# Optimization experiments

Measured on AMD Instinct MI355X. Metric: run time of the kernel, lower is better.

The kernel has to match this reference:

```python
import jax, jax.numpy as jnp
import numpy as np

D_MODEL = 1024
N_HEAD = 16
HEAD_DIM = D_MODEL // N_HEAD


def setup_inputs() -> dict:
    key = jax.random.key(0)
    k1, k2, k3 = jax.random.split(key, 3)
    B, T = 2, 2048
    x = jax.random.normal(k1, (B, T, D_MODEL), dtype=jnp.float32)
    # nn.MultiheadAttention packed in-projection: (3*D, D), xavier-like scale
    w_in = jax.random.normal(k2, (3 * D_MODEL, D_MODEL), dtype=jnp.float32) * (1.0 / np.sqrt(D_MODEL))
    b_in = jnp.zeros((3 * D_MODEL,), dtype=jnp.float32)
    w_out = jax.random.normal(k3, (D_MODEL, D_MODEL), dtype=jnp.float32) * (1.0 / np.sqrt(D_MODEL))
    b_out = jnp.zeros((D_MODEL,), dtype=jnp.float32)
    return {"x": x, "w_in": w_in, "b_in": b_in, "w_out": w_out, "b_out": b_out}


def reference(x, w_in, b_in, w_out, b_out):
    B, T, D = x.shape
    H, hd = N_HEAD, HEAD_DIM
    # packed QKV projection (torch Linear convention: y = x @ W.T + b)
    qkv = x @ w_in.T + b_in                      # [B, T, 3D]
    q, k, v = jnp.split(qkv, 3, axis=-1)
    # [B, H, T, hd]
    q = q.reshape(B, T, H, hd).transpose(0, 2, 1, 3)
    k = k.reshape(B, T, H, hd).transpose(0, 2, 1, 3)
    v = v.reshape(B, T, H, hd).transpose(0, 2, 1, 3)
    scale = 1.0 / np.sqrt(hd).astype(np.float32)
    scores = jnp.einsum("bhqd,bhkd->bhqk", q * scale, k)  # [B, H, T, T]
    causal = jnp.tril(jnp.ones((T, T), dtype=bool))
    scores = jnp.where(causal, scores, jnp.finfo(scores.dtype).min)
    attn = jax.nn.softmax(scores, axis=-1)
    ctx = jnp.einsum("bhqk,bhkd->bhqd", attn, v)           # [B, H, T, hd]
    ctx = ctx.transpose(0, 2, 1, 3).reshape(B, T, D)
    return ctx @ w_out.T + b_out
```

## Files before the change

### kernel.cpp

```cpp
#include <hip/hip_runtime.h>


#define T_SEQ 2048
#define D_MODEL 1024
#define NEG_BIG (-1.0e30f)
#define Q_SCALE 0.18033688f

typedef float f32x4 __attribute__((ext_vector_type(4)));
typedef short s16x8 __attribute__((ext_vector_type(8)));
typedef __bf16 bf16x8 __attribute__((ext_vector_type(8)));

__device__ __forceinline__ f32x4 mfma16(s16x8 a, s16x8 b, f32x4 c) {
    return __builtin_amdgcn_mfma_f32_16x16x32_bf16(
        __builtin_bit_cast(bf16x8, a), __builtin_bit_cast(bf16x8, b), c, 0, 0, 0);
}

__device__ __forceinline__ short f2bf(float f) {
    unsigned int u = __float_as_uint(f);
    u += 0x7fffu + ((u >> 16) & 1u);
    return (short)(u >> 16);
}
__device__ __forceinline__ unsigned f2bfu(float f) {
    unsigned int u = __float_as_uint(f);
    u += 0x7fffu + ((u >> 16) & 1u);
    return u >> 16;
}
__device__ __forceinline__ unsigned f2bfu_fast(float f) {
    return (__float_as_uint(f) + 0x8000u) >> 16;
}
__device__ __forceinline__ float bf2f(short s) {
    return __uint_as_float(((unsigned int)(unsigned short)s) << 16);
}

__device__ __forceinline__ void async_lds16(const short* g, short* l) {
    __builtin_amdgcn_global_load_lds(
        (const __attribute__((address_space(1))) unsigned int*)g,
        (__attribute__((address_space(3))) unsigned int*)l, 16, 0, 0);
}

#define N_X   4194304
#define N_WI  3145728
#define N_BI  3072
#define N_WO  1048576
#define N_BO  1024
#define V_X   (N_X  / 4)
#define V_WI  (N_WI / 4)
#define V_BI  (N_BI / 4)
#define V_WO  (N_WO / 4)
#define V_BO  (N_BO / 4)
#define V_TOT (V_X + V_WI + V_BI + V_WO + V_BO)

__global__ __launch_bounds__(256) void canon_all_kernel(
    const float* __restrict__ x, const float* __restrict__ wi,
    const float* __restrict__ bi, const float* __restrict__ wo,
    const float* __restrict__ bo,
    short* __restrict__ xb, short* __restrict__ wib, short* __restrict__ bib,
    short* __restrict__ wob, short* __restrict__ bob)
{
    int i = blockIdx.x * 256 + threadIdx.x;
    if (i >= V_TOT) return;
    const float* src; short* dst; int off;
    if      (i < V_X)                    { src = x;  dst = xb;  off = i; }
    else if (i < V_X+V_WI)               { src = wi; dst = wib; off = i - V_X; }
    else if (i < V_X+V_WI+V_BI)          { src = bi; dst = bib; off = i - V_X - V_WI; }
    else if (i < V_X+V_WI+V_BI+V_WO)     { src = wo; dst = wob; off = i - V_X - V_WI - V_BI; }
    else                                 { src = bo; dst = bob; off = i - V_X - V_WI - V_BI - V_WO; }
    float4 v = ((const float4*)src)[off];
    short4 o = { f2bf(v.x), f2bf(v.y), f2bf(v.z), f2bf(v.w) };
    ((short4*)dst)[off] = o;
}

__global__ __launch_bounds__(256) void gemm_qkv_kernel(
    const short* __restrict__ A, const short* __restrict__ B,
    const short* __restrict__ bias,
    short* __restrict__ qo, short* __restrict__ ko, short* __restrict__ vto)
{
    const int K = 1024;
    alignas(16) __shared__ short As[128][32];
    alignas(16) __shared__ short Bs[128][32];
    const int m0 = blockIdx.x * 128;
    const int n0 = blockIdx.y * 128;
    const int tid = threadIdx.x;
    const int lane = tid & 63;
    const int w = tid >> 6;
    const int wm = (w >> 1) * 64, wn = (w & 1) * 64;
    const int quad = lane >> 4, l16 = lane & 15;

    f32x4 acc[4][4];
    const f32x4 zero = {0.f, 0.f, 0.f, 0.f};
#pragma unroll
    for (int i = 0; i < 4; ++i)
#pragma unroll
        for (int j = 0; j < 4; ++j) acc[i][j] = zero;

    const int lrow = lane >> 2;
    const int lcol = (lane & 3) * 8;
    const short* gA0 = &A[(m0 + w*32      + lrow) * K + lcol];
    const short* gA1 = &A[(m0 + w*32 + 16 + lrow) * K + lcol];
    const short* gB0 = &B[(n0 + w*32      + lrow) * K + lcol];
    const short* gB1 = &B[(n0 + w*32 + 16 + lrow) * K + lcol];
    short* lA0 = &As[w*32][0];
    short* lA1 = &As[w*32 + 16][0];
    short* lB0 = &Bs[w*32][0];
    short* lB1 = &Bs[w*32 + 16][0];

    for (int k0 = 0; k0 < K; k0 += 32) {
        __syncthreads();
        async_lds16(gA0 + k0, lA0);
        async_lds16(gA1 + k0, lA1);
        async_lds16(gB0 + k0, lB0);
        async_lds16(gB1 + k0, lB1);
        __syncthreads();

        s16x8 af[4], bfr[4];
#pragma unroll
        for (int i = 0; i < 4; ++i) af[i]  = *(const s16x8*)&As[wm + i*16 + l16][quad*8];
#pragma unroll
        for (int j = 0; j < 4; ++j) bfr[j] = *(const s16x8*)&Bs[wn + j*16 + l16][quad*8];
#pragma unroll
        for (int i = 0; i < 4; ++i)
#pragma unroll
            for (int j = 0; j < 4; ++j)
                acc[i][j] = mfma16(af[i], bfr[j], acc[i][j]);
    }

#pragma unroll
    for (int j = 0; j < 4; ++j) {
        int n = n0 + wn + j*16 + l16;
        float bi = bf2f(bias[n]);
        int which = n >> 10;
        int h = (n >> 6) & 15, d = n & 63;
        if (which < 2) {
            short* dst = (which == 0) ? qo : ko;
            float scl = (which == 0) ? Q_SCALE : 1.0f;
#pragma unroll
            for (int i = 0; i < 4; ++i) {
#pragma unroll
                for (int r = 0; r < 4; ++r) {
                    int m = m0 + wm + i*16 + quad*4 + r;
                    int b = m >> 11, t = m & 2047;
                    float v = (acc[i][j][r] + bi) * scl;
                    dst[(((b*16 + h) * 2048) + t) * 64 + d] = f2bf(v);
                }
            }
        } else {
#pragma unroll
            for (int i = 0; i < 4; ++i) {
                int m = m0 + wm + i*16 + quad*4;
                int b = m >> 11, t0 = m & 2047;
                short4 o4 = { f2bf(acc[i][j][0] + bi), f2bf(acc[i][j][1] + bi),
                              f2bf(acc[i][j][2] + bi), f2bf(acc[i][j][3] + bi) };
                *(short4*)&vto[(((size_t)(b*16 + h) * 64) + d) * 2048 + t0] = o4;
            }
        }
    }
}

__global__ __launch_bounds__(256) void attn_kernel(
    const short* __restrict__ Q, const short* __restrict__ K,
    const short* __restrict__ Vt, short* __restrict__ ctx)
{
    alignas(16) __shared__ short Ks[64][72];
    alignas(16) __shared__ short Vs[64][72];
    alignas(16) __shared__ short Pl[4][16][72];

    const int id = blockIdx.x;
    const int kk = id >> 8;
    const int r8 = id & 255;
    const int a  = r8 & 15;
    const int bhl = r8 >> 4;
    int qt, bh;
    if      (kk == 0) { qt = a;      bh = bhl;      }
    else if (kk == 1) { qt = 31 - a; bh = bhl;      }
    else if (kk == 2) { qt = 15 - a; bh = 16 + bhl; }
    else              { qt = 16 + a; bh = 16 + bhl; }

    const int qbase = qt * 64;
    const int tid = threadIdx.x;
    const int w = tid >> 6, lane = tid & 63;
    const int quad = lane >> 4, l16 = lane & 15;
    const int b = bh >> 4, h = bh & 15;

    const short* Qb  = Q  + bh * T_SEQ * 64;
    const short* Kb  = K  + bh * T_SEQ * 64;
    const short* Vbt = Vt + (size_t)bh * 64 * T_SEQ;

    const short* qrow = Qb + (qbase + w*16 + l16) * 64;
    const s16x8 qa0 = *(const s16x8*)(qrow + quad*8);
    const s16x8 qa1 = *(const s16x8*)(qrow + 32 + quad*8);

    const f32x4 zero = {0.f, 0.f, 0.f, 0.f};
    f32x4 o[4];
#pragma unroll
    for (int dt = 0; dt < 4; ++dt) o[dt] = zero;
    float lsum = 0.f;

    const int sr  = tid >> 3;
    const int scl = (tid & 7) * 8;
    const int qg  = qbase + w*16 + l16;

    float4 kf0 = *(const float4*)&Kb[sr * 64 + scl];
    float4 kf1 = *(const float4*)&Kb[(sr + 32) * 64 + scl];
    float4 vf0 = *(const float4*)&Vbt[(size_t)sr * T_SEQ + scl];
    float4 vf1 = *(const float4*)&Vbt[(size_t)(sr + 32) * T_SEQ + scl];

    for (int s0 = 0; s0 <= qbase; s0 += 64) {
        __syncthreads();
        *(float4*)&Ks[sr][scl]    = kf0;
        *(float4*)&Ks[sr+32][scl] = kf1;
        *(float4*)&Vs[sr][scl]    = vf0;
        *(float4*)&Vs[sr+32][scl] = vf1;
        __syncthreads();

        if (s0 + 64 <= qbase) {
            kf0 = *(const float4*)&Kb[(s0 + 64 + sr) * 64 + scl];
            kf1 = *(const float4*)&Kb[(s0 + 64 + sr + 32) * 64 + scl];
            vf0 = *(const float4*)&Vbt[(size_t)sr * T_SEQ + s0 + 64 + scl];
            vf1 = *(const float4*)&Vbt[(size_t)(sr + 32) * T_SEQ + s0 + 64 + scl];
        }

#pragma unroll
        for (int sub = 0; sub < 4; ++sub) {
            s16x8 ka0 = *(const s16x8*)&Ks[sub*16 + l16][quad*8];
            s16x8 ka1 = *(const s16x8*)&Ks[sub*16 + l16][32 + quad*8];
            f32x4 S = mfma16(ka1, qa1, mfma16(ka0, qa0, zero));
            if (s0 == qbase) {
                int sb = s0 + sub*16 + quad*4;
#pragma unroll
                for (int r = 0; r < 4; ++r)
                    if (sb + r > qg) S[r] = NEG_BIG;
            }
            float p0 = exp2f(S[0]), p1 = exp2f(S[1]);
            float p2 = exp2f(S[2]), p3 = exp2f(S[3]);
            lsum += (p0 + p1) + (p2 + p3);
            uint2 pk;
            pk.x = f2bfu_fast(p0) | (f2bfu_fast(p1) << 16);
            pk.y = f2bfu_fast(p2) | (f2bfu_fast(p3) << 16);
            *(uint2*)&Pl[w][l16][sub*16 + quad*4] = pk;
        }

        s16x8 pb0 = *(const s16x8*)&Pl[w][l16][quad*8];
        s16x8 pb1 = *(const s16x8*)&Pl[w][l16][32 + quad*8];
#pragma unroll
        for (int dt = 0; dt < 4; ++dt) {
            s16x8 va0 = *(const s16x8*)&Vs[dt*16 + l16][quad*8];
            s16x8 va1 = *(const s16x8*)&Vs[dt*16 + l16][32 + quad*8];
            o[dt] = mfma16(va1, pb1, mfma16(va0, pb0, o[dt]));
        }
    }

    lsum += __shfl_xor(lsum, 16, 64);
    lsum += __shfl_xor(lsum, 32, 64);
    float inv = 1.0f / lsum;
    int base = (b * T_SEQ + qg) * D_MODEL + h * 64;
#pragma unroll
    for (int dt = 0; dt < 4; ++dt) {
        uint2 pk;
        pk.x = f2bfu(o[dt][0] * inv) | (f2bfu(o[dt][1] * inv) << 16);
        pk.y = f2bfu(o[dt][2] * inv) | (f2bfu(o[dt][3] * inv) << 16);
        *(uint2*)&ctx[base + dt*16 + quad*4] = pk;
    }
}

__global__ __launch_bounds__(256) void gemm_out_kernel(
    const short* __restrict__ A, const short* __restrict__ B,
    const short* __restrict__ bias, float* __restrict__ out)
{
    const int K = 1024;
    alignas(16) __shared__ short As[128][32];
    alignas(16) __shared__ short Bs[64][32];
    const int m0 = blockIdx.x * 128;
    const int n0 = blockIdx.y * 64;
    const int tid = threadIdx.x;
    const int lane = tid & 63;
    const int w = tid >> 6;
    const int wm = (w >> 1) * 64, wn = (w & 1) * 32;
    const int quad = lane >> 4, l16 = lane & 15;

    f32x4 acc[4][2];
    const f32x4 zero = {0.f, 0.f, 0.f, 0.f};
#pragma unroll
    for (int i = 0; i < 4; ++i)
#pragma unroll
        for (int j = 0; j < 2; ++j) acc[i][j] = zero;

    const int lrow = lane >> 2;
    const int lcol = (lane & 3) * 8;
    const short* gA0 = &A[(m0 + w*32      + lrow) * K + lcol];
    const short* gA1 = &A[(m0 + w*32 + 16 + lrow) * K + lcol];
    const short* gB0 = &B[(n0 + w*16 + lrow) * K + lcol];
    short* lA0 = &As[w*32][0];
    short* lA1 = &As[w*32 + 16][0];
    short* lB0 = &Bs[w*16][0];

    for (int k0 = 0; k0 < K; k0 += 32) {
        __syncthreads();
        async_lds16(gA0 + k0, lA0);
        async_lds16(gA1 + k0, lA1);
        async_lds16(gB0 + k0, lB0);
        __syncthreads();

        s16x8 af[4], bfr[2];
#pragma unroll
        for (int i = 0; i < 4; ++i) af[i]  = *(const s16x8*)&As[wm + i*16 + l16][quad*8];
#pragma unroll
        for (int j = 0; j < 2; ++j) bfr[j] = *(const s16x8*)&Bs[wn + j*16 + l16][quad*8];
#pragma unroll
        for (int i = 0; i < 4; ++i)
#pragma unroll
            for (int j = 0; j < 2; ++j)
                acc[i][j] = mfma16(af[i], bfr[j], acc[i][j]);
    }

#pragma unroll
    for (int j = 0; j < 2; ++j) {
        int n = n0 + wn + j*16 + l16;
        float bi = bf2f(bias[n]);
#pragma unroll
        for (int i = 0; i < 4; ++i) {
#pragma unroll
            for (int r = 0; r < 4; ++r) {
                int m = m0 + wm + i*16 + quad*4 + r;
                out[m * 1024 + n] = acc[i][j][r] + bi;
            }
        }
    }
}

extern "C" void kernel_launch(void* const* d_in, const int* in_sizes, int n_in,
                              void* d_out, int out_size, void* d_ws, size_t ws_size,
                              hipStream_t stream) {
    float* out = (float*)d_out;
    char* ws = (char*)d_ws;

    const size_t MB = 1u << 20;
    short* xb     = (short*)(ws);
    short* w_inb  = (short*)(ws + 8*MB);
    short* b_inb  = (short*)(ws + 14*MB);
    short* w_outb = (short*)(ws + 15*MB);
    short* b_outb = (short*)(ws + 17*MB);
    short* qb     = (short*)(ws + 18*MB);
    short* kb     = (short*)(ws + 26*MB);
    short* vtb    = (short*)(ws + 34*MB);
    short* ctxb   = (short*)(ws + 42*MB);

    canon_all_kernel<<<(V_TOT + 255) / 256, 256, 0, stream>>>(
        (const float*)d_in[0], (const float*)d_in[1], (const float*)d_in[2],
        (const float*)d_in[3], (const float*)d_in[4],
        xb, w_inb, b_inb, w_outb, b_outb);

    gemm_qkv_kernel<<<dim3(32, 24), 256, 0, stream>>>(xb, w_inb, b_inb, qb, kb, vtb);
    attn_kernel<<<dim3(1024), 256, 0, stream>>>(qb, kb, vtb, ctxb);
    gemm_out_kernel<<<dim3(32, 16), 256, 0, stream>>>(ctxb, w_outb, b_outb, out);
}
```

Baseline: 184.2 us.

## Double K-step in GEMMs, reorder attention grid, use hardware bf16 pack

Both GEMM kernels now load two 32-wide K slices per iteration into separate LDS buffers, halving the number of barrier pairs and loop iterations. The attention grid changes from a hand-balanced 1D mapping to a 2D grid that issues the longest causal query tiles first. Float-to-bf16 packing switches to the v_cvt_pk_bf16_f32 instruction instead of integer bit tricks. The trade-offs are more LDS use per GEMM block and a changed load-balance pattern in attention.

```diff
diff --git a/kernel.cpp b/kernel.cpp
--- a/kernel.cpp
+++ b/kernel.cpp
@@ -20,16 +20,13 @@
     u += 0x7fffu + ((u >> 16) & 1u);
     return (short)(u >> 16);
 }
-__device__ __forceinline__ unsigned f2bfu(float f) {
-    unsigned int u = __float_as_uint(f);
-    u += 0x7fffu + ((u >> 16) & 1u);
-    return u >> 16;
-}
-__device__ __forceinline__ unsigned f2bfu_fast(float f) {
-    return (__float_as_uint(f) + 0x8000u) >> 16;
-}
 __device__ __forceinline__ float bf2f(short s) {
     return __uint_as_float(((unsigned int)(unsigned short)s) << 16);
+}
+__device__ __forceinline__ unsigned cvt_pk_bf16(float lo, float hi) {
+    unsigned r;
+    asm("v_cvt_pk_bf16_f32 %0, %1, %2" : "=v"(r) : "v"(lo), "v"(hi));
+    return r;
 }
 
 __device__ __forceinline__ void async_lds16(const short* g, short* l) {
@@ -76,8 +73,10 @@
     short* __restrict__ qo, short* __restrict__ ko, short* __restrict__ vto)
 {
     const int K = 1024;
-    alignas(16) __shared__ short As[128][32];
-    alignas(16) __shared__ short Bs[128][32];
+    alignas(16) __shared__ short As0[128][32];
+    alignas(16) __shared__ short As1[128][32];
+    alignas(16) __shared__ short Bs0[128][32];
+    alignas(16) __shared__ short Bs1[128][32];
     const int m0 = blockIdx.x * 128;
     const int n0 = blockIdx.y * 128;
     const int tid = threadIdx.x;
@@ -95,28 +94,49 @@
 
     const int lrow = lane >> 2;
     const int lcol = (lane & 3) * 8;
-    const short* gA0 = &A[(m0 + w*32      + lrow) * K + lcol];
-    const short* gA1 = &A[(m0 + w*32 + 16 + lrow) * K + lcol];
-    const short* gB0 = &B[(n0 + w*32      + lrow) * K + lcol];
-    const short* gB1 = &B[(n0 + w*32 + 16 + lrow) * K + lcol];
-    short* lA0 = &As[w*32][0];
-    short* lA1 = &As[w*32 + 16][0];
-    short* lB0 = &Bs[w*32][0];
-    short* lB1 = &Bs[w*32 + 16][0];
-
-    for (int k0 = 0; k0 < K; k0 += 32) {
-        __syncthreads();
-        async_lds16(gA0 + k0, lA0);
-        async_lds16(gA1 + k0, lA1);
-        async_lds16(gB0 + k0, lB0);
-        async_lds16(gB1 + k0, lB1);
+    const short* gA00 = &A[(m0 + w*32      + lrow) * K + lcol];
+    const short* gA01 = &A[(m0 + w*32 + 16 + lrow) * K + lcol];
+    const short* gA10 = gA00 + 32;
+    const short* gA11 = gA01 + 32;
+    const short* gB00 = &B[(n0 + w*32      + lrow) * K + lcol];
+    const short* gB01 = &B[(n0 + w*32 + 16 + lrow) * K + lcol];
+    const short* gB10 = gB00 + 32;
+    const short* gB11 = gB01 + 32;
+    short* lA00 = &As0[w*32][0];
+    short* lA01 = &As0[w*32 + 16][0];
+    short* lA10 = &As1[w*32][0];
+    short* lA11 = &As1[w*32 + 16][0];
+    short* lB00 = &Bs0[w*32][0];
+    short* lB01 = &Bs0[w*32 + 16][0];
+    short* lB10 = &Bs1[w*32][0];
+    short* lB11 = &Bs1[w*32 + 16][0];
+
+    for (int k0 = 0; k0 < K; k0 += 64) {
+        __syncthreads();
+        async_lds16(gA00 + k0, lA00);
+        async_lds16(gA01 + k0, lA01);
+        async_lds16(gA10 + k0, lA10);
+        async_lds16(gA11 + k0, lA11);
+        async_lds16(gB00 + k0, lB00);
+        async_lds16(gB01 + k0, lB01);
+        async_lds16(gB10 + k0, lB10);
+        async_lds16(gB11 + k0, lB11);
         __syncthreads();
 
         s16x8 af[4], bfr[4];
 #pragma unroll
-        for (int i = 0; i < 4; ++i) af[i]  = *(const s16x8*)&As[wm + i*16 + l16][quad*8];
-#pragma unroll
-        for (int j = 0; j < 4; ++j) bfr[j] = *(const s16x8*)&Bs[wn + j*16 + l16][quad*8];
+        for (int i = 0; i < 4; ++i) af[i]  = *(const s16x8*)&As0[wm + i*16 + l16][quad*8];
+#pragma unroll
+        for (int j = 0; j < 4; ++j) bfr[j] = *(const s16x8*)&Bs0[wn + j*16 + l16][quad*8];
+#pragma unroll
+        for (int i = 0; i < 4; ++i)
+#pragma unroll
+            for (int j = 0; j < 4; ++j)
+                acc[i][j] = mfma16(af[i], bfr[j], acc[i][j]);
+#pragma unroll
+        for (int i = 0; i < 4; ++i) af[i]  = *(const s16x8*)&As1[wm + i*16 + l16][quad*8];
+#pragma unroll
+        for (int j = 0; j < 4; ++j) bfr[j] = *(const s16x8*)&Bs1[wn + j*16 + l16][quad*8];
 #pragma unroll
         for (int i = 0; i < 4; ++i)
 #pragma unroll
@@ -164,17 +184,8 @@
     alignas(16) __shared__ short Vs[64][72];
     alignas(16) __shared__ short Pl[4][16][72];
 
-    const int id = blockIdx.x;
-    const int kk = id >> 8;
-    const int r8 = id & 255;
-    const int a  = r8 & 15;
-    const int bhl = r8 >> 4;
-    int qt, bh;
-    if      (kk == 0) { qt = a;      bh = bhl;      }
-    else if (kk == 1) { qt = 31 - a; bh = bhl;      }
-    else if (kk == 2) { qt = 15 - a; bh = 16 + bhl; }
-    else              { qt = 16 + a; bh = 16 + bhl; }
-
+    const int bh = blockIdx.x;
+    const int qt = 31 - (int)blockIdx.y;
     const int qbase = qt * 64;
     const int tid = threadIdx.x;
     const int w = tid >> 6, lane = tid & 63;
@@ -234,8 +245,8 @@
             float p2 = exp2f(S[2]), p3 = exp2f(S[3]);
             lsum += (p0 + p1) + (p2 + p3);
             uint2 pk;
-            pk.x = f2bfu_fast(p0) | (f2bfu_fast(p1) << 16);
-            pk.y = f2bfu_fast(p2) | (f2bfu_fast(p3) << 16);
+            pk.x = cvt_pk_bf16(p0, p1);
+            pk.y = cvt_pk_bf16(p2, p3);
             *(uint2*)&Pl[w][l16][sub*16 + quad*4] = pk;
         }
 
@@ -256,8 +267,8 @@
 #pragma unroll
     for (int dt = 0; dt < 4; ++dt) {
         uint2 pk;
-        pk.x = f2bfu(o[dt][0] * inv) | (f2bfu(o[dt][1] * inv) << 16);
-        pk.y = f2bfu(o[dt][2] * inv) | (f2bfu(o[dt][3] * inv) << 16);
+        pk.x = cvt_pk_bf16(o[dt][0] * inv, o[dt][1] * inv);
+        pk.y = cvt_pk_bf16(o[dt][2] * inv, o[dt][3] * inv);
         *(uint2*)&ctx[base + dt*16 + quad*4] = pk;
     }
 }
@@ -267,8 +278,10 @@
     const short* __restrict__ bias, float* __restrict__ out)
 {
     const int K = 1024;
-    alignas(16) __shared__ short As[128][32];
-    alignas(16) __shared__ short Bs[64][32];
+    alignas(16) __shared__ short As0[128][32];
+    alignas(16) __shared__ short As1[128][32];
+    alignas(16) __shared__ short Bs0[64][32];
+    alignas(16) __shared__ short Bs1[64][32];
     const int m0 = blockIdx.x * 128;
     const int n0 = blockIdx.y * 64;
     const int tid = threadIdx.x;
@@ -286,25 +299,43 @@
 
     const int lrow = lane >> 2;
     const int lcol = (lane & 3) * 8;
-    const short* gA0 = &A[(m0 + w*32      + lrow) * K + lcol];
-    const short* gA1 = &A[(m0 + w*32 + 16 + lrow) * K + lcol];
-    const short* gB0 = &B[(n0 + w*16 + lrow) * K + lcol];
-    short* lA0 = &As[w*32][0];
-    short* lA1 = &As[w*32 + 16][0];
-    short* lB0 = &Bs[w*16][0];
-
-    for (int k0 = 0; k0 < K; k0 += 32) {
-        __syncthreads();
-        async_lds16(gA0 + k0, lA0);
-        async_lds16(gA1 + k0, lA1);
-        async_lds16(gB0 + k0, lB0);
+    const short* gA00 = &A[(m0 + w*32      + lrow) * K + lcol];
+    const short* gA01 = &A[(m0 + w*32 + 16 + lrow) * K + lcol];
+    const short* gA10 = gA00 + 32;
+    const short* gA11 = gA01 + 32;
+    const short* gB00 = &B[(n0 + w*16 + lrow) * K + lcol];
+    const short* gB10 = gB00 + 32;
+    short* lA00 = &As0[w*32][0];
+    short* lA01 = &As0[w*32 + 16][0];
+    short* lA10 = &As1[w*32][0];
+    short* lA11 = &As1[w*32 + 16][0];
+    short* lB00 = &Bs0[w*16][0];
+    short* lB10 = &Bs1[w*16][0];
+
+    for (int k0 = 0; k0 < K; k0 += 64) {
+        __syncthreads();
+        async_lds16(gA00 + k0, lA00);
+        async_lds16(gA01 + k0, lA01);
+        async_lds16(gA10 + k0, lA10);
+        async_lds16(gA11 + k0, lA11);
+        async_lds16(gB00 + k0, lB00);
+        async_lds16(gB10 + k0, lB10);
         __syncthreads();
 
         s16x8 af[4], bfr[2];
 #pragma unroll
-        for (int i = 0; i < 4; ++i) af[i]  = *(const s16x8*)&As[wm + i*16 + l16][quad*8];
-#pragma unroll
-        for (int j = 0; j < 2; ++j) bfr[j] = *(const s16x8*)&Bs[wn + j*16 + l16][quad*8];
+        for (int i = 0; i < 4; ++i) af[i]  = *(const s16x8*)&As0[wm + i*16 + l16][quad*8];
+#pragma unroll
+        for (int j = 0; j < 2; ++j) bfr[j] = *(const s16x8*)&Bs0[wn + j*16 + l16][quad*8];
+#pragma unroll
+        for (int i = 0; i < 4; ++i)
+#pragma unroll
+            for (int j = 0; j < 2; ++j)
+                acc[i][j] = mfma16(af[i], bfr[j], acc[i][j]);
+#pragma unroll
+        for (int i = 0; i < 4; ++i) af[i]  = *(const s16x8*)&As1[wm + i*16 + l16][quad*8];
+#pragma unroll
+        for (int j = 0; j < 2; ++j) bfr[j] = *(const s16x8*)&Bs1[wn + j*16 + l16][quad*8];
 #pragma unroll
         for (int i = 0; i < 4; ++i)
 #pragma unroll
@@ -350,6 +381,6 @@
         xb, w_inb, b_inb, w_outb, b_outb);
 
     gemm_qkv_kernel<<<dim3(32, 24), 256, 0, stream>>>(xb, w_inb, b_inb, qb, kb, vtb);
-    attn_kernel<<<dim3(1024), 256, 0, stream>>>(qb, kb, vtb, ctxb);
+    attn_kernel<<<dim3(32, 32), 256, 0, stream>>>(qb, kb, vtb, ctxb);
     gemm_out_kernel<<<dim3(32, 16), 256, 0, stream>>>(ctxb, w_outb, b_outb, out);
 }
```

Result: no change. 182.4 us (-1.0%).
